# Kernel optimization log

Hardware: AMD Instinct MI355X
Metric: run time of the kernel (lower is better)

The kernel has to match this reference:

```python
import jax, jax.numpy as jnp
import numpy as np

TEMP = 10.0  # softmax temperature (self.Temp)
N_CENTERS = 16

def setup_inputs() -> dict:
    key = jax.random.key(0)
    k1, k2 = jax.random.split(key)
    x = jax.random.normal(k1, (16, 64, 128, 128), dtype=jnp.float32)
    center = jax.random.normal(k2, (N_CENTERS,), dtype=jnp.float32)
    return {"x": x, "center": center}

def reference(x, center):
    # Soft quantization branch (Q_type='Soft') with straight-through estimator.
    # diff[..., m] = x - center[m]  (broadcast instead of torch.stack)
    diff = x[..., None] - center  # [*, K]
    W_index = jnp.argmin(jnp.abs(diff), axis=-1)  # [*]
    W_hard = center[W_index]  # [*]
    smx = jax.nn.softmax(-TEMP * diff * diff, axis=-1)  # [*, K]
    W_soft = jnp.einsum('ijklm,m->ijkl', smx, center)  # [*]
    w_bias = jax.lax.stop_gradient(W_hard - W_soft)
    return w_bias + W_soft
```

## Files before the change

### kernel.cpp

```cpp
#include <hip/hip_runtime.h>
#include <hip/hip_bf16.h>
#include <math.h>

#define N_CENTERS 16
#define B_LUT 1024


__global__ void build_lut_kernel(const float* __restrict__ center,
                                 float* __restrict__ ws)
{
    int t = blockIdx.x * blockDim.x + threadIdx.x;
    if (t >= B_LUT) return;

    float s[N_CENTERS];
#pragma unroll
    for (int m = 0; m < N_CENTERS; ++m) s[m] = center[m];
#pragma unroll
    for (int a = 0; a < N_CENTERS - 1; ++a)
#pragma unroll
        for (int j = 0; j < N_CENTERS - 1 - a; ++j) {
            float u = fminf(s[j], s[j + 1]);
            float v = fmaxf(s[j], s[j + 1]);
            s[j] = u; s[j + 1] = v;
        }

    float lo = s[0], hi = s[N_CENTERS - 1];
    float span = hi - lo;
    if (!(span > 0.f)) span = 1.f;
    float w = span / (float)B_LUT;
    float invw = (float)B_LUT / span;
    float nb = -lo * invw;

    if (t == 0) { ws[0] = lo; ws[1] = invw; ws[2] = nb; ws[3] = 0.f; }
    float2* lut = (float2*)(ws + 4);

    float mid[N_CENTERS - 1];
#pragma unroll
    for (int j = 0; j < N_CENTERS - 1; ++j) mid[j] = 0.5f * (s[j] + s[j + 1]);

    float bstart = lo + t * w;
    float bend = bstart + w;
    float g = 0.02f * w;

    int cnt = 0, j0 = 0;
#pragma unroll
    for (int j = 0; j < N_CENTERS - 1; ++j) {
        bool inb = (mid[j] >= bstart - g) && (mid[j] < bend + g);
        if (inb) { if (cnt == 0) j0 = j; cnt++; }
    }

    float ca, cb;
    if (cnt == 0) {
        int k = 0;
#pragma unroll
        for (int j = 0; j < N_CENTERS - 1; ++j) k += (mid[j] < bstart) ? 1 : 0;
        float ck = s[0];
#pragma unroll
        for (int j = 1; j < N_CENTERS; ++j) ck = (j == k) ? s[j] : ck;
        ca = ck; cb = ck;
    } else if (cnt == 1) {
        float a = s[0], b = s[1];
#pragma unroll
        for (int j = 0; j < N_CENTERS - 1; ++j)
            if (j == j0) { a = s[j]; b = s[j + 1]; }
        int ia = N_CENTERS - 1, ib = N_CENTERS - 1;
#pragma unroll
        for (int m = N_CENTERS - 1; m >= 0; --m) {
            float cm = center[m];
            if (cm == a) ia = m;
            if (cm == b) ib = m;
        }
        if (ia <= ib) { ca = a; cb = b; } else { ca = b; cb = a; }
    } else {
        ca = __uint_as_float(0x7fc00000u);
        cb = 0.f;
    }
    lut[t] = make_float2(ca, cb);
}

__global__ void __launch_bounds__(256) quantizer_kernel(
    const float* __restrict__ x,
    const float* __restrict__ center,
    const float* __restrict__ ws,
    float* __restrict__ out,
    int q)
{
    __shared__ __align__(16) float2 slut[B_LUT];

    const float4* __restrict__ x4 = reinterpret_cast<const float4*>(x);
    float4* __restrict__ o4 = reinterpret_cast<float4*>(out);

    int i = blockIdx.x * blockDim.x + threadIdx.x;

    float4 v0 = x4[i];
    float4 v1 = x4[i + q];
    float4 v2 = x4[i + 2 * q];
    float4 v3 = x4[i + 3 * q];

    const float4* __restrict__ g4 = reinterpret_cast<const float4*>(ws + 4);
    float4* s4 = reinterpret_cast<float4*>(slut);
    s4[threadIdx.x] = g4[threadIdx.x];
    s4[threadIdx.x + 256] = g4[threadIdx.x + 256];

    float invw = ws[1];
    float nb = ws[2];
    __syncthreads();

    float xs[16] = {v0.x, v0.y, v0.z, v0.w, v1.x, v1.y, v1.z, v1.w,
                    v2.x, v2.y, v2.z, v2.w, v3.x, v3.y, v3.z, v3.w};

    float r[16];
    bool bad = false;
#pragma unroll
    for (int j = 0; j < 16; ++j) {
        float ft = fmaf(xs[j], invw, nb);
        ft = __builtin_amdgcn_fmed3f(ft, 0.f, (float)(B_LUT - 1));
        int t = (int)ft;
        float2 e = slut[t];
        float da = fabsf(xs[j] - e.x);
        float db = fabsf(xs[j] - e.y);
        r[j] = (db < da) ? e.y : e.x;
        bad |= (e.x != e.x);
    }

    if (__any(bad)) {
#pragma unroll
        for (int j = 0; j < 16; ++j) {
            float xv = xs[j];
            float best = fabsf(xv - center[0]);
            float bc = center[0];
#pragma unroll
            for (int m = 1; m < N_CENTERS; ++m) {
                float d = fabsf(xv - center[m]);
                bool lt = d < best;
                best = lt ? d : best;
                bc = lt ? center[m] : bc;
            }
            r[j] = bc;
        }
    }

    o4[i]         = make_float4(r[0],  r[1],  r[2],  r[3]);
    o4[i + q]     = make_float4(r[4],  r[5],  r[6],  r[7]);
    o4[i + 2 * q] = make_float4(r[8],  r[9],  r[10], r[11]);
    o4[i + 3 * q] = make_float4(r[12], r[13], r[14], r[15]);
}

extern "C" void kernel_launch(void* const* d_in, const int* in_sizes, int n_in,
                              void* d_out, int out_size, void* d_ws, size_t ws_size,
                              hipStream_t stream) {
    const float* x      = (const float*)d_in[0];
    const float* center = (const float*)d_in[1];
    float* out          = (float*)d_out;
    float* ws           = (float*)d_ws;

    int n = in_sizes[0];
    int n4 = n / 4;
    int q  = n4 / 4;

    build_lut_kernel<<<B_LUT / 256, 256, 0, stream>>>(center, ws);

    const int block = 256;
    int grid = q / block;
    quantizer_kernel<<<grid, block, 0, stream>>>(x, center, ws, out, q);
}
```

Baseline: 30.67 us.

## Fuse LUT construction into quantizer kernel with smaller per-block LUT

Removes the separate LUT-building launch and workspace round-trip by having each block sort the centers and build a 256-entry lookup table directly in shared memory. The LUT shrinks so each thread fills one entry. Outputs are written with nontemporal stores, and the exact fallback reloads x and overwrites the outputs when any lane hits an ambiguous bin. Every block now redoes the 16-element sort and LUT build, and coarser bins make the exact fallback more likely.

```diff
diff --git a/kernel.cpp b/kernel.cpp
--- a/kernel.cpp
+++ b/kernel.cpp
@@ -3,14 +3,72 @@
 #include <math.h>
 
 #define N_CENTERS 16
-#define B_LUT 1024
+#define B_LUT 256
+
+typedef float nfloat4 __attribute__((ext_vector_type(4)));
 
 
-__global__ void build_lut_kernel(const float* __restrict__ center,
-                                 float* __restrict__ ws)
+__device__ __forceinline__ void quant4(const float4 v,
+                                       const float2* __restrict__ slut,
+                                       float invw, float nb,
+                                       nfloat4& rr, bool& bad)
 {
-    int t = blockIdx.x * blockDim.x + threadIdx.x;
-    if (t >= B_LUT) return;
+    float xs[4] = {v.x, v.y, v.z, v.w};
+    float r[4];
+#pragma unroll
+    for (int j = 0; j < 4; ++j) {
+        float ft = fmaf(xs[j], invw, nb);
+        ft = __builtin_amdgcn_fmed3f(ft, 0.f, (float)(B_LUT - 1));
+        int t = (int)ft;
+        float2 e = slut[t];
+        float da = fabsf(xs[j] - e.x);
+        float db = fabsf(xs[j] - e.y);
+        r[j] = (db < da) ? e.y : e.x;
+        bad |= (e.x != e.x);
+    }
+    rr = (nfloat4){r[0], r[1], r[2], r[3]};
+}
+
+__device__ __forceinline__ float4 exact4(const float4 v,
+                                         const float* __restrict__ center)
+{
+    float xs[4] = {v.x, v.y, v.z, v.w};
+    float r[4];
+#pragma unroll
+    for (int j = 0; j < 4; ++j) {
+        float xv = xs[j];
+        float best = fabsf(xv - center[0]);
+        float bc = center[0];
+#pragma unroll
+        for (int m = 1; m < N_CENTERS; ++m) {
+            float d = fabsf(xv - center[m]);
+            bool lt = d < best;
+            best = lt ? d : best;
+            bc = lt ? center[m] : bc;
+        }
+        r[j] = bc;
+    }
+    return make_float4(r[0], r[1], r[2], r[3]);
+}
+
+__global__ void __launch_bounds__(256) quantizer_kernel(
+    const float* __restrict__ x,
+    const float* __restrict__ center,
+    float* __restrict__ out,
+    int q)
+{
+    __shared__ __align__(16) float2 slut[B_LUT];
+
+    const float4* __restrict__ x4 = reinterpret_cast<const float4*>(x);
+    float4* __restrict__ o4 = reinterpret_cast<float4*>(out);
+    nfloat4* __restrict__ o4n = reinterpret_cast<nfloat4*>(out);
+
+    int i = blockIdx.x * blockDim.x + threadIdx.x;
+
+    float4 v0 = x4[i];
+    float4 v1 = x4[i + q];
+    float4 v2 = x4[i + 2 * q];
+    float4 v3 = x4[i + 3 * q];
 
     float s[N_CENTERS];
 #pragma unroll
@@ -20,8 +78,8 @@
 #pragma unroll
         for (int j = 0; j < N_CENTERS - 1 - a; ++j) {
             float u = fminf(s[j], s[j + 1]);
-            float v = fmaxf(s[j], s[j + 1]);
-            s[j] = u; s[j + 1] = v;
+            float vmx = fmaxf(s[j], s[j + 1]);
+            s[j] = u; s[j + 1] = vmx;
         }
 
     float lo = s[0], hi = s[N_CENTERS - 1];
@@ -31,119 +89,75 @@
     float invw = (float)B_LUT / span;
     float nb = -lo * invw;
 
-    if (t == 0) { ws[0] = lo; ws[1] = invw; ws[2] = nb; ws[3] = 0.f; }
-    float2* lut = (float2*)(ws + 4);
+    {
+        int t = threadIdx.x;
+        float bstart = lo + t * w;
+        float bend = bstart + w;
+        float g = 0.02f * w;
 
-    float mid[N_CENTERS - 1];
+        float mid[N_CENTERS - 1];
 #pragma unroll
-    for (int j = 0; j < N_CENTERS - 1; ++j) mid[j] = 0.5f * (s[j] + s[j + 1]);
+        for (int j = 0; j < N_CENTERS - 1; ++j) mid[j] = 0.5f * (s[j] + s[j + 1]);
 
-    float bstart = lo + t * w;
-    float bend = bstart + w;
-    float g = 0.02f * w;
+        int cnt = 0, j0 = 0;
+#pragma unroll
+        for (int j = 0; j < N_CENTERS - 1; ++j) {
+            bool inb = (mid[j] >= bstart - g) && (mid[j] < bend + g);
+            if (inb) { if (cnt == 0) j0 = j; cnt++; }
+        }
 
-    int cnt = 0, j0 = 0;
+        float ca, cb;
+        if (cnt == 0) {
+            int k = 0;
 #pragma unroll
-    for (int j = 0; j < N_CENTERS - 1; ++j) {
-        bool inb = (mid[j] >= bstart - g) && (mid[j] < bend + g);
-        if (inb) { if (cnt == 0) j0 = j; cnt++; }
+            for (int j = 0; j < N_CENTERS - 1; ++j) k += (mid[j] < bstart) ? 1 : 0;
+            float ck = s[0];
+#pragma unroll
+            for (int j = 1; j < N_CENTERS; ++j) ck = (j == k) ? s[j] : ck;
+            ca = ck; cb = ck;
+        } else if (cnt == 1) {
+            float a = s[0], b = s[1];
+#pragma unroll
+            for (int j = 0; j < N_CENTERS - 1; ++j)
+                if (j == j0) { a = s[j]; b = s[j + 1]; }
+            int ia = N_CENTERS - 1, ib = N_CENTERS - 1;
+#pragma unroll
+            for (int m = N_CENTERS - 1; m >= 0; --m) {
+                float cm = center[m];
+                if (cm == a) ia = m;
+                if (cm == b) ib = m;
+            }
+            if (ia <= ib) { ca = a; cb = b; } else { ca = b; cb = a; }
+        } else {
+            ca = __uint_as_float(0x7fc00000u);
+            cb = 0.f;
+        }
+        slut[t] = make_float2(ca, cb);
     }
-
-    float ca, cb;
-    if (cnt == 0) {
-        int k = 0;
-#pragma unroll
-        for (int j = 0; j < N_CENTERS - 1; ++j) k += (mid[j] < bstart) ? 1 : 0;
-        float ck = s[0];
-#pragma unroll
-        for (int j = 1; j < N_CENTERS; ++j) ck = (j == k) ? s[j] : ck;
-        ca = ck; cb = ck;
-    } else if (cnt == 1) {
-        float a = s[0], b = s[1];
-#pragma unroll
-        for (int j = 0; j < N_CENTERS - 1; ++j)
-            if (j == j0) { a = s[j]; b = s[j + 1]; }
-        int ia = N_CENTERS - 1, ib = N_CENTERS - 1;
-#pragma unroll
-        for (int m = N_CENTERS - 1; m >= 0; --m) {
-            float cm = center[m];
-            if (cm == a) ia = m;
-            if (cm == b) ib = m;
-        }
-        if (ia <= ib) { ca = a; cb = b; } else { ca = b; cb = a; }
-    } else {
-        ca = __uint_as_float(0x7fc00000u);
-        cb = 0.f;
-    }
-    lut[t] = make_float2(ca, cb);
-}
-
-__global__ void __launch_bounds__(256) quantizer_kernel(
-    const float* __restrict__ x,
-    const float* __restrict__ center,
-    const float* __restrict__ ws,
-    float* __restrict__ out,
-    int q)
-{
-    __shared__ __align__(16) float2 slut[B_LUT];
-
-    const float4* __restrict__ x4 = reinterpret_cast<const float4*>(x);
-    float4* __restrict__ o4 = reinterpret_cast<float4*>(out);
-
-    int i = blockIdx.x * blockDim.x + threadIdx.x;
-
-    float4 v0 = x4[i];
-    float4 v1 = x4[i + q];
-    float4 v2 = x4[i + 2 * q];
-    float4 v3 = x4[i + 3 * q];
-
-    const float4* __restrict__ g4 = reinterpret_cast<const float4*>(ws + 4);
-    float4* s4 = reinterpret_cast<float4*>(slut);
-    s4[threadIdx.x] = g4[threadIdx.x];
-    s4[threadIdx.x + 256] = g4[threadIdx.x + 256];
-
-    float invw = ws[1];
-    float nb = ws[2];
     __syncthreads();
 
-    float xs[16] = {v0.x, v0.y, v0.z, v0.w, v1.x, v1.y, v1.z, v1.w,
-                    v2.x, v2.y, v2.z, v2.w, v3.x, v3.y, v3.z, v3.w};
+    bool bad = false;
+    nfloat4 r0, r1, r2, r3;
+    quant4(v0, slut, invw, nb, r0, bad);
+    quant4(v1, slut, invw, nb, r1, bad);
+    quant4(v2, slut, invw, nb, r2, bad);
+    quant4(v3, slut, invw, nb, r3, bad);
 
-    float r[16];
-    bool bad = false;
-#pragma unroll
-    for (int j = 0; j < 16; ++j) {
-        float ft = fmaf(xs[j], invw, nb);
-        ft = __builtin_amdgcn_fmed3f(ft, 0.f, (float)(B_LUT - 1));
-        int t = (int)ft;
-        float2 e = slut[t];
-        float da = fabsf(xs[j] - e.x);
-        float db = fabsf(xs[j] - e.y);
-        r[j] = (db < da) ? e.y : e.x;
-        bad |= (e.x != e.x);
-    }
+    __builtin_nontemporal_store(r0, &o4n[i]);
+    __builtin_nontemporal_store(r1, &o4n[i + q]);
+    __builtin_nontemporal_store(r2, &o4n[i + 2 * q]);
+    __builtin_nontemporal_store(r3, &o4n[i + 3 * q]);
 
     if (__any(bad)) {
-#pragma unroll
-        for (int j = 0; j < 16; ++j) {
-            float xv = xs[j];
-            float best = fabsf(xv - center[0]);
-            float bc = center[0];
-#pragma unroll
-            for (int m = 1; m < N_CENTERS; ++m) {
-                float d = fabsf(xv - center[m]);
-                bool lt = d < best;
-                best = lt ? d : best;
-                bc = lt ? center[m] : bc;
-            }
-            r[j] = bc;
-        }
+        float4 e0 = exact4(x4[i], center);
+        float4 e1 = exact4(x4[i + q], center);
+        float4 e2 = exact4(x4[i + 2 * q], center);
+        float4 e3 = exact4(x4[i + 3 * q], center);
+        o4[i]         = e0;
+        o4[i + q]     = e1;
+        o4[i + 2 * q] = e2;
+        o4[i + 3 * q] = e3;
     }
-
-    o4[i]         = make_float4(r[0],  r[1],  r[2],  r[3]);
-    o4[i + q]     = make_float4(r[4],  r[5],  r[6],  r[7]);
-    o4[i + 2 * q] = make_float4(r[8],  r[9],  r[10], r[11]);
-    o4[i + 3 * q] = make_float4(r[12], r[13], r[14], r[15]);
 }
 
 extern "C" void kernel_launch(void* const* d_in, const int* in_sizes, int n_in,
@@ -152,15 +166,12 @@
     const float* x      = (const float*)d_in[0];
     const float* center = (const float*)d_in[1];
     float* out          = (float*)d_out;
-    float* ws           = (float*)d_ws;
 
     int n = in_sizes[0];
     int n4 = n / 4;
     int q  = n4 / 4;
 
-    build_lut_kernel<<<B_LUT / 256, 256, 0, stream>>>(center, ws);
-
     const int block = 256;
     int grid = q / block;
-    quantizer_kernel<<<grid, block, 0, stream>>>(x, center, ws, out, q);
+    quantizer_kernel<<<grid, block, 0, stream>>>(x, center, out, q);
 }
```

Result: faster. 27.90 us (-9.0%).
